# Optimization experiments

Measured on AMD Instinct MI355X. Metric: run time of the kernel, lower is better.

## Reference

```python
import jax, jax.numpy as jnp
import numpy as np

B, IN, H = 8192, 1024, 2048

def setup_inputs() -> dict:
    key = jax.random.key(0)
    ks = jax.random.split(key, 9)
    s_g = 1.0 / np.sqrt(IN + H)
    s_r = 1.0 / np.sqrt(IN)
    return {
        "x_t": jax.random.normal(ks[0], (B, IN), jnp.float32),
        "h_t_1": jax.random.normal(ks[1], (B, H), jnp.float32),
        "c_t_1": jax.random.normal(ks[2], (B, H), jnp.float32),
        # stacked gate weights [4, IN+H, H] in order (input, forget, output, c_hat)
        "W_gates": jax.random.uniform(ks[3], (4, IN + H, H), jnp.float32, -s_g, s_g),
        "b_gates": jax.random.uniform(ks[4], (4, H), jnp.float32, -s_g, s_g),
        "W_res": jax.random.uniform(ks[5], (IN, H), jnp.float32, -s_r, s_r),
        "b_res": jax.random.uniform(ks[6], (H,), jnp.float32, -s_r, s_r),
    }

def reference(x_t, h_t_1, c_t_1, W_gates, b_gates, W_res, b_res):
    xh = jnp.concatenate([x_t, h_t_1], axis=1)            # [B, IN+H]
    # one batched GEMM for all 4 gates: [B, IN+H] x [4, IN+H, H] -> [4, B, H]
    gates = jnp.einsum('bk,gkh->gbh', xh, W_gates) + b_gates[:, None, :]
    i_t = jax.nn.sigmoid(gates[0])
    f_t = jax.nn.sigmoid(gates[1])
    o_t = jax.nn.sigmoid(gates[2])
    c_hat = jnp.tanh(gates[3])
    c_t = f_t * c_t_1 + i_t * c_hat
    x_res = x_t @ W_res + b_res                            # input_size != hidden_size
    h_t = o_t * jnp.tanh(c_t) + x_res
    return h_t, c_t
```

## Files before the change

kernel.cpp:

```cpp
#include <hip/hip_runtime.h>
#include <cstdint>
#include <cstddef>

#define Bsz 8192
#define INsz 1024
#define Hsz 2048
#define Kxh 3072

typedef __attribute__((ext_vector_type(8))) short bf16x8;
typedef __attribute__((ext_vector_type(4))) float f32x4;

__device__ __forceinline__ unsigned short f2bf(float f) {
  unsigned int u = __float_as_uint(f);
  u += 0x7FFFu + ((u >> 16) & 1u);
  return (unsigned short)(u >> 16);
}

__device__ __forceinline__ void gload_lds16(const void* g, void* l) {
  __builtin_amdgcn_global_load_lds(
      (const __attribute__((address_space(1))) void*)g,
      (__attribute__((address_space(3))) void*)l, 16, 0, 0);
}

__device__ __forceinline__ float fsigmoid(float x) { return 1.f / (1.f + __expf(-x)); }
__device__ __forceinline__ float ftanh(float x) {
  float ax = fabsf(x);
  float t = __expf(-2.f * ax);
  float r = (1.f - t) / (1.f + t);
  return copysignf(r, x);
}

__global__ void convert_xh_kernel(const float* __restrict__ x,
                                  const float* __restrict__ h,
                                  unsigned short* __restrict__ xh) {
  int chunk = blockIdx.x * 256 + threadIdx.x;
  int row = chunk / 384;
  int c8 = (chunk - row * 384) * 8;
  const float* src = (c8 < INsz) ? (x + (size_t)row * INsz + c8)
                                 : (h + (size_t)row * Hsz + (c8 - INsz));
  f32x4 v0 = *(const f32x4*)src;
  f32x4 v1 = *(const f32x4*)(src + 4);
  bf16x8 o;
  o[0] = (short)f2bf(v0[0]); o[1] = (short)f2bf(v0[1]);
  o[2] = (short)f2bf(v0[2]); o[3] = (short)f2bf(v0[3]);
  o[4] = (short)f2bf(v1[0]); o[5] = (short)f2bf(v1[1]);
  o[6] = (short)f2bf(v1[2]); o[7] = (short)f2bf(v1[3]);
  *(bf16x8*)(xh + (size_t)chunk * 8) = o;
}

__global__ void transpose_conv_kernel(const float* __restrict__ W,
                                      unsigned short* __restrict__ WT,
                                      int K, int N) {
  __shared__ float tile[32][33];
  const size_t moff = (size_t)blockIdx.z * (size_t)K * N;
  const float* Wg = W + moff;
  unsigned short* WTg = WT + moff;
  int n0 = blockIdx.x * 32;
  int k0 = blockIdx.y * 32;
  int tx = threadIdx.x, ty = threadIdx.y;
  #pragma unroll
  for (int j = 0; j < 4; ++j)
    tile[ty + j * 8][tx] = Wg[(size_t)(k0 + ty + j * 8) * N + n0 + tx];
  __syncthreads();
  #pragma unroll
  for (int j = 0; j < 4; ++j)
    WTg[(size_t)(n0 + ty + j * 8) * K + k0 + tx] = f2bf(tile[tx][ty + j * 8]);
}

__device__ __forceinline__ void gemm_pass(
    const unsigned short* __restrict__ A,
    const unsigned short* __restrict__ Bt,
    int ldb, int K,
    short* lA, short* lB,
    int tid, int lane, int wr, int wc,
    f32x4 (&acc)[4][4])
{
  const int il = lane & 15;
  const int kl = (lane >> 4) * 8;
  for (int k0 = 0; k0 < K; k0 += 64) {
    #pragma unroll
    for (int c = 0; c < 4; ++c) {
      int ch = c * 256 + tid;
      int row = ch >> 3;
      int col = (ch & 7) * 8;
      gload_lds16(A + (size_t)row * Kxh + k0 + col, lA + ch * 8);
    }
    #pragma unroll
    for (int c = 0; c < 4; ++c) {
      int ch = c * 256 + tid;
      int row = ch >> 3;
      int col = (ch & 7) * 8;
      gload_lds16(Bt + (size_t)row * ldb + k0 + col, lB + ch * 8);
    }
    __syncthreads();
    #pragma unroll
    for (int ks = 0; ks < 2; ++ks) {
      bf16x8 a[4], b[4];
      #pragma unroll
      for (int m = 0; m < 4; ++m)
        a[m] = *(const bf16x8*)&lA[(wr * 64 + m * 16 + il) * 64 + ks * 32 + kl];
      #pragma unroll
      for (int n = 0; n < 4; ++n)
        b[n] = *(const bf16x8*)&lB[(wc * 64 + n * 16 + il) * 64 + ks * 32 + kl];
      #pragma unroll
      for (int m = 0; m < 4; ++m)
        #pragma unroll
        for (int n = 0; n < 4; ++n)
          acc[m][n] = __builtin_amdgcn_mfma_f32_16x16x32_bf16(a[m], b[n], acc[m][n], 0, 0, 0);
    }
    __syncthreads();
  }
}

__global__ __launch_bounds__(256, 2) void lstm_fused_kernel(
    const unsigned short* __restrict__ xh,
    const unsigned short* __restrict__ WgT,
    const unsigned short* __restrict__ WrT,
    const float* __restrict__ c_prev,
    const float* __restrict__ b_gates,
    const float* __restrict__ b_res,
    float* __restrict__ h_out,
    float* __restrict__ c_out)
{
  __shared__ alignas(16) short lA[128 * 64];
  __shared__ alignas(16) short lB[128 * 64];
  const int tid = threadIdx.x;
  const int lane = tid & 63;
  const int wid = tid >> 6;
  const int wr = wid >> 1, wc = wid & 1;
  const int brow = (blockIdx.x >> 4) * 128;
  const int bcol = (blockIdx.x & 15) * 128;

  const unsigned short* Ab = xh + (size_t)brow * Kxh;
  const int col0 = bcol + wc * 64 + (lane & 15);
  const int row0 = brow + wr * 64 + ((lane >> 4) << 2);

  const f32x4 zf = {0.f, 0.f, 0.f, 0.f};
  f32x4 acc[4][4];
  f32x4 C[4][4];
  f32x4 I[4][4];

  #pragma unroll
  for (int m = 0; m < 4; ++m)
    #pragma unroll
    for (int n = 0; n < 4; ++n) acc[m][n] = zf;
  gemm_pass(Ab, WgT + (size_t)(1 * Hsz + bcol) * Kxh, Kxh, Kxh, lA, lB, tid, lane, wr, wc, acc);
  #pragma unroll
  for (int n = 0; n < 4; ++n) {
    float bgn = b_gates[1 * Hsz + col0 + n * 16];
    #pragma unroll
    for (int m = 0; m < 4; ++m)
      #pragma unroll
      for (int r = 0; r < 4; ++r) {
        float f = fsigmoid(acc[m][n][r] + bgn);
        C[m][n][r] = f * c_prev[(size_t)(row0 + m * 16 + r) * Hsz + col0 + n * 16];
      }
  }

  #pragma unroll
  for (int m = 0; m < 4; ++m)
    #pragma unroll
    for (int n = 0; n < 4; ++n) acc[m][n] = zf;
  gemm_pass(Ab, WgT + (size_t)(0 * Hsz + bcol) * Kxh, Kxh, Kxh, lA, lB, tid, lane, wr, wc, acc);
  #pragma unroll
  for (int n = 0; n < 4; ++n) {
    float bgn = b_gates[0 * Hsz + col0 + n * 16];
    #pragma unroll
    for (int m = 0; m < 4; ++m)
      #pragma unroll
      for (int r = 0; r < 4; ++r)
        I[m][n][r] = fsigmoid(acc[m][n][r] + bgn);
  }

  #pragma unroll
  for (int m = 0; m < 4; ++m)
    #pragma unroll
    for (int n = 0; n < 4; ++n) acc[m][n] = zf;
  gemm_pass(Ab, WgT + (size_t)(3 * Hsz + bcol) * Kxh, Kxh, Kxh, lA, lB, tid, lane, wr, wc, acc);
  #pragma unroll
  for (int n = 0; n < 4; ++n) {
    float bgn = b_gates[3 * Hsz + col0 + n * 16];
    #pragma unroll
    for (int m = 0; m < 4; ++m)
      #pragma unroll
      for (int r = 0; r < 4; ++r) {
        float ct = C[m][n][r] + I[m][n][r] * ftanh(acc[m][n][r] + bgn);
        c_out[(size_t)(row0 + m * 16 + r) * Hsz + col0 + n * 16] = ct;
        C[m][n][r] = ftanh(ct);
      }
  }

  #pragma unroll
  for (int m = 0; m < 4; ++m)
    #pragma unroll
    for (int n = 0; n < 4; ++n) acc[m][n] = zf;
  gemm_pass(Ab, WgT + (size_t)(2 * Hsz + bcol) * Kxh, Kxh, Kxh, lA, lB, tid, lane, wr, wc, acc);
  #pragma unroll
  for (int n = 0; n < 4; ++n) {
    float bgn = b_gates[2 * Hsz + col0 + n * 16];
    #pragma unroll
    for (int m = 0; m < 4; ++m)
      #pragma unroll
      for (int r = 0; r < 4; ++r)
        C[m][n][r] = fsigmoid(acc[m][n][r] + bgn) * C[m][n][r];
  }

  #pragma unroll
  for (int m = 0; m < 4; ++m)
    #pragma unroll
    for (int n = 0; n < 4; ++n) acc[m][n] = zf;
  gemm_pass(Ab, WrT + (size_t)bcol * INsz, INsz, INsz, lA, lB, tid, lane, wr, wc, acc);
  #pragma unroll
  for (int n = 0; n < 4; ++n) {
    float brn = b_res[col0 + n * 16];
    #pragma unroll
    for (int m = 0; m < 4; ++m)
      #pragma unroll
      for (int r = 0; r < 4; ++r)
        h_out[(size_t)(row0 + m * 16 + r) * Hsz + col0 + n * 16] =
            C[m][n][r] + acc[m][n][r] + brn;
  }
}

extern "C" void kernel_launch(void* const* d_in, const int* in_sizes, int n_in,
                              void* d_out, int out_size, void* d_ws, size_t ws_size,
                              hipStream_t stream) {
  const float* x  = (const float*)d_in[0];
  const float* h  = (const float*)d_in[1];
  const float* c  = (const float*)d_in[2];
  const float* Wg = (const float*)d_in[3];
  const float* bg = (const float*)d_in[4];
  const float* Wr = (const float*)d_in[5];
  const float* br = (const float*)d_in[6];
  float* out = (float*)d_out;

  char* ws = (char*)d_ws;
  unsigned short* xh  = (unsigned short*)ws;
  unsigned short* WgT = (unsigned short*)(ws + 50331648);
  unsigned short* WrT = (unsigned short*)(ws + 100663296);

  convert_xh_kernel<<<12288, 256, 0, stream>>>(x, h, xh);
  transpose_conv_kernel<<<dim3(64, 96, 4), dim3(32, 8), 0, stream>>>(Wg, WgT, Kxh, Hsz);
  transpose_conv_kernel<<<dim3(64, 32, 1), dim3(32, 8), 0, stream>>>(Wr, WrT, INsz, Hsz);

  lstm_fused_kernel<<<1024, 256, 0, stream>>>(
      xh, WgT, WrT, c, bg, br, out, out + (size_t)Bsz * Hsz);
}
```

Measured before the change: 1.054 ms.

## Swizzle LDS tiles, remap workgroups for XCD locality, vectorize weight transpose

Applies an XOR swizzle to the LDS layout of the A and B tiles so that MFMA fragment reads avoid bank conflicts. Remaps workgroup IDs so that blocks landing on the same XCD share column tiles of the weights, which is meant to improve L2 reuse. Rewrites the weight transpose-convert kernel to use 64x64 tiles with vectorized float4 loads and 16-byte bf16 stores. The swizzle mapping must match between the global-to-LDS loads and the fragment reads, and the remap assumes a round-robin dispatch across 8 XCDs.

```diff
diff --git a/kernel.cpp b/kernel.cpp
--- a/kernel.cpp
+++ b/kernel.cpp
@@ -51,20 +51,33 @@
 __global__ void transpose_conv_kernel(const float* __restrict__ W,
                                       unsigned short* __restrict__ WT,
                                       int K, int N) {
-  __shared__ float tile[32][33];
+  __shared__ float tile[64][65];
   const size_t moff = (size_t)blockIdx.z * (size_t)K * N;
-  const float* Wg = W + moff;
-  unsigned short* WTg = WT + moff;
-  int n0 = blockIdx.x * 32;
-  int k0 = blockIdx.y * 32;
-  int tx = threadIdx.x, ty = threadIdx.y;
-  #pragma unroll
-  for (int j = 0; j < 4; ++j)
-    tile[ty + j * 8][tx] = Wg[(size_t)(k0 + ty + j * 8) * N + n0 + tx];
+  int n0 = blockIdx.x * 64;
+  int k0 = blockIdx.y * 64;
+  int t = threadIdx.x;
+  #pragma unroll
+  for (int j = 0; j < 4; ++j) {
+    int idx = j * 256 + t;
+    int row = idx >> 4;
+    int c4 = (idx & 15) * 4;
+    f32x4 v = *(const f32x4*)&W[moff + (size_t)(k0 + row) * N + n0 + c4];
+    tile[row][c4 + 0] = v[0];
+    tile[row][c4 + 1] = v[1];
+    tile[row][c4 + 2] = v[2];
+    tile[row][c4 + 3] = v[3];
+  }
   __syncthreads();
   #pragma unroll
-  for (int j = 0; j < 4; ++j)
-    WTg[(size_t)(n0 + ty + j * 8) * K + k0 + tx] = f2bf(tile[tx][ty + j * 8]);
+  for (int j = 0; j < 2; ++j) {
+    int idx = j * 256 + t;
+    int nr = idx >> 3;
+    int kc = (idx & 7) * 8;
+    bf16x8 o;
+    #pragma unroll
+    for (int i = 0; i < 8; ++i) o[i] = (short)f2bf(tile[kc + i][nr]);
+    *(bf16x8*)&WT[moff + (size_t)(n0 + nr) * K + k0 + kc] = o;
+  }
 }
 
 __device__ __forceinline__ void gemm_pass(
@@ -77,20 +90,21 @@
 {
   const int il = lane & 15;
   const int kl = (lane >> 4) * 8;
+  const int axor = (il & 7) << 3;
   for (int k0 = 0; k0 < K; k0 += 64) {
     #pragma unroll
     for (int c = 0; c < 4; ++c) {
       int ch = c * 256 + tid;
       int row = ch >> 3;
-      int col = (ch & 7) * 8;
-      gload_lds16(A + (size_t)row * Kxh + k0 + col, lA + ch * 8);
+      int scc = (ch & 7) ^ (row & 7);
+      gload_lds16(A + (size_t)row * Kxh + k0 + scc * 8, lA + ch * 8);
     }
     #pragma unroll
     for (int c = 0; c < 4; ++c) {
       int ch = c * 256 + tid;
       int row = ch >> 3;
-      int col = (ch & 7) * 8;
-      gload_lds16(Bt + (size_t)row * ldb + k0 + col, lB + ch * 8);
+      int scc = (ch & 7) ^ (row & 7);
+      gload_lds16(Bt + (size_t)row * ldb + k0 + scc * 8, lB + ch * 8);
     }
     __syncthreads();
     #pragma unroll
@@ -98,10 +112,10 @@
       bf16x8 a[4], b[4];
       #pragma unroll
       for (int m = 0; m < 4; ++m)
-        a[m] = *(const bf16x8*)&lA[(wr * 64 + m * 16 + il) * 64 + ks * 32 + kl];
+        a[m] = *(const bf16x8*)&lA[(wr * 64 + m * 16 + il) * 64 + ((ks * 32 + kl) ^ axor)];
       #pragma unroll
       for (int n = 0; n < 4; ++n)
-        b[n] = *(const bf16x8*)&lB[(wc * 64 + n * 16 + il) * 64 + ks * 32 + kl];
+        b[n] = *(const bf16x8*)&lB[(wc * 64 + n * 16 + il) * 64 + ((ks * 32 + kl) ^ axor)];
       #pragma unroll
       for (int m = 0; m < 4; ++m)
         #pragma unroll
@@ -128,8 +142,11 @@
   const int lane = tid & 63;
   const int wid = tid >> 6;
   const int wr = wid >> 1, wc = wid & 1;
-  const int brow = (blockIdx.x >> 4) * 128;
-  const int bcol = (blockIdx.x & 15) * 128;
+
+  const int orig = blockIdx.x;
+  const int wg = (orig & 7) * 128 + (orig >> 3);
+  const int bcol = (wg >> 6) * 128;
+  const int brow = (wg & 63) * 128;
 
   const unsigned short* Ab = xh + (size_t)brow * Kxh;
   const int col0 = bcol + wc * 64 + (lane & 15);
@@ -240,8 +257,8 @@
   unsigned short* WrT = (unsigned short*)(ws + 100663296);
 
   convert_xh_kernel<<<12288, 256, 0, stream>>>(x, h, xh);
-  transpose_conv_kernel<<<dim3(64, 96, 4), dim3(32, 8), 0, stream>>>(Wg, WgT, Kxh, Hsz);
-  transpose_conv_kernel<<<dim3(64, 32, 1), dim3(32, 8), 0, stream>>>(Wr, WrT, INsz, Hsz);
+  transpose_conv_kernel<<<dim3(32, 48, 4), 256, 0, stream>>>(Wg, WgT, Kxh, Hsz);
+  transpose_conv_kernel<<<dim3(32, 16, 1), 256, 0, stream>>>(Wr, WrT, INsz, Hsz);
 
   lstm_fused_kernel<<<1024, 256, 0, stream>>>(
       xh, WgT, WrT, c, bg, br, out, out + (size_t)Bsz * Hsz);
```

Measured after the change: 1.011 ms. -4.1%, faster.
